# Kernel optimization log

Hardware: AMD Instinct MI355X
Metric: run time of the kernel (lower is better)

The kernel has to match this reference:

```python
import jax, jax.numpy as jnp
import numpy as np

N_NODES = 100000
N_EDGES = 1600000
IN_CH = 128
HID = 128
OUT_CH = 10
NUM_LAYERS = 3
NUM_GRAPHS = 512


def _glorot(key, shape):
    fan_in, fan_out = shape[0], shape[1]
    lim = jnp.sqrt(6.0 / (fan_in + fan_out))
    return jax.random.uniform(key, shape, jnp.float32, -lim, lim)


def setup_inputs() -> dict:
    key = jax.random.key(0)
    ks = jax.random.split(key, 20)
    inp = {}
    inp["x"] = jax.random.normal(ks[0], (N_NODES, IN_CH), jnp.float32)
    inp["edge_index"] = jax.random.randint(ks[1], (2, N_EDGES), 0, N_NODES, jnp.int64)
    inp["batch"] = jnp.sort(jax.random.randint(ks[2], (N_NODES,), 0, NUM_GRAPHS, jnp.int64))
    # GIN layer MLP params: Linear(in, hid) -> ReLU -> Linear(hid, hid)
    kidx = 3
    for l in range(NUM_LAYERS):
        d_in = IN_CH if l == 0 else HID
        inp[f"w1_{l}"] = _glorot(ks[kidx], (d_in, HID)); kidx += 1
        inp[f"b1_{l}"] = jnp.zeros((HID,), jnp.float32)
        inp[f"w2_{l}"] = _glorot(ks[kidx], (HID, HID)); kidx += 1
        inp[f"b2_{l}"] = jnp.zeros((HID,), jnp.float32)
    inp["lin_w"] = _glorot(ks[kidx], (HID, OUT_CH))
    inp["lin_b"] = jnp.zeros((OUT_CH,), jnp.float32)
    return inp


def _gin_forward(x, src, dst, batch, layer_params, lin_w, lin_b):
    h = x
    n_layers = len(layer_params)
    for i, (w1, b1, w2, b2) in enumerate(layer_params):
        # GINConv: (1 + eps) * h + sum_{j in N(i)} h_j, eps = 0
        agg = jax.ops.segment_sum(h[src], dst, num_segments=N_NODES)
        z = h + agg
        # MLP: Linear -> ReLU -> Linear
        h = jnp.maximum(z @ w1 + b1, 0.0) @ w2 + b2
        if i < n_layers - 1:  # inter-layer ReLU (PyG BasicGNN act)
            h = jnp.maximum(h, 0.0)
    # global_add_pool over batch ids -> [NUM_GRAPHS, HID]
    pooled = jax.ops.segment_sum(h, batch, num_segments=NUM_GRAPHS)
    # dropout(p=0.5) is identity in eval mode
    return pooled @ lin_w + lin_b


def reference(x, edge_index, batch,
              w1_0, b1_0, w2_0, b2_0,
              w1_1, b1_1, w2_1, b2_1,
              w1_2, b1_2, w2_2, b2_2,
              lin_w, lin_b):
    src, dst = edge_index[0], edge_index[1]
    layer_params = [(w1_0, b1_0, w2_0, b2_0),
                    (w1_1, b1_1, w2_1, b2_1),
                    (w1_2, b1_2, w2_2, b2_2)]
    return _gin_forward(x, src, dst, batch, layer_params, lin_w, lin_b)
```

## Files before the change

### kernel.cpp

```cpp
#include <hip/hip_runtime.h>

#define CH 128
#define OUTC 10
#define NB 256
#define BCAP 10240
#define PCHUNK 2048
#define PQ2 132
#define FBM 64

typedef __attribute__((ext_vector_type(8))) short short8;
typedef __attribute__((ext_vector_type(4))) short short4v;
typedef __attribute__((ext_vector_type(16))) float f32x16;


__device__ inline unsigned short f2bf(float f) {
    unsigned u = __builtin_bit_cast(unsigned, f);
    u += 0x7fffu + ((u >> 16) & 1u);
    return (unsigned short)(u >> 16);
}
__device__ inline float bflo(unsigned u) { return __builtin_bit_cast(float, u << 16); }
__device__ inline float bfhi(unsigned u) { return __builtin_bit_cast(float, u & 0xffff0000u); }

__device__ inline void acc8(float* a, const uint4& v) {
    a[0] += bflo(v.x); a[1] += bfhi(v.x);
    a[2] += bflo(v.y); a[3] += bfhi(v.y);
    a[4] += bflo(v.z); a[5] += bfhi(v.z);
    a[6] += bflo(v.w); a[7] += bfhi(v.w);
}


struct WPtrs { const float* s[6]; unsigned short* d[6]; };

__global__ void prep_part_kernel(const int* __restrict__ src, const int* __restrict__ dst,
                                 int* __restrict__ bucketCnt, unsigned* __restrict__ pairs, int E,
                                 int nPartBlk,
                                 const float4* __restrict__ x4, uint2* __restrict__ xb, int n4,
                                 int nConvBlk, WPtrs p,
                                 uint4* __restrict__ pooled4, int nPooled4) {
    __shared__ int hist[NB];
    __shared__ int base[NB];
    __shared__ int cur[NB];
    int tid = threadIdx.x;
    int b = blockIdx.x;

    if (b < nPartBlk) {
        int e0 = b * PCHUNK;
        hist[tid] = 0;
        __syncthreads();
        #pragma unroll
        for (int i = 0; i < PCHUNK / 256; ++i) {
            int e = e0 + tid + i * 256;
            if (e < E) atomicAdd(&hist[dst[e] >> 9], 1);
        }
        __syncthreads();
        {
            int c = hist[tid];
            base[tid] = (c > 0) ? atomicAdd(&bucketCnt[tid], c) : 0;
            cur[tid] = 0;
        }
        __syncthreads();
        #pragma unroll
        for (int i = 0; i < PCHUNK / 256; ++i) {
            int e = e0 + tid + i * 256;
            if (e < E) {
                int d = dst[e];
                int bkt = d >> 9;
                int pos = base[bkt] + atomicAdd(&cur[bkt], 1);
                if (pos < BCAP)
                    pairs[bkt * BCAP + pos] = ((unsigned)(d & 511) << 17) | (unsigned)src[e];
            }
        }
    } else if (b < nPartBlk + nConvBlk) {
        int i = (b - nPartBlk) * 256 + tid;
        if (i < n4) {
            float4 v = x4[i];
            uint2 o;
            o.x = (unsigned)f2bf(v.x) | ((unsigned)f2bf(v.y) << 16);
            o.y = (unsigned)f2bf(v.z) | ((unsigned)f2bf(v.w) << 16);
            xb[i] = o;
        }
    } else if (b < nPartBlk + nConvBlk + 384) {
        int bb = b - nPartBlk - nConvBlk;
        int m = bb >> 6;
        int i = (bb & 63) * 256 + tid;
        int j = i & 7;
        int l = (i >> 3) & 63;
        int k0 = (i >> 9) & 7;
        int ct = (i >> 12) & 3;
        int k = k0 * 16 + ((l >> 5) << 3) + j;
        int nn = ct * 32 + (l & 31);
        p.d[m][i] = f2bf(p.s[m][k * CH + nn]);
    } else {
        int i = (b - nPartBlk - nConvBlk - 384) * 256 + tid;
        if (i < nPooled4) pooled4[i] = make_uint4(0, 0, 0, 0);
    }
}


__launch_bounds__(256)
__global__ void build_csr_kernel(const unsigned* __restrict__ pairs, const int* __restrict__ bucketCnt,
                                 int* __restrict__ offs, int* __restrict__ csr, int N) {
    __shared__ int bsm[NB];
    __shared__ int ldeg[512];
    __shared__ int s0[512], s1[512];
    __shared__ int lexc[512];
    __shared__ int lcur[512];
    __shared__ int lcsr[BCAP];

    int b = blockIdx.x;
    int node0 = b << 9;
    if (node0 >= N) return;
    int nLocal = min(512, N - node0);
    int tid = threadIdx.x;

    bsm[tid] = bucketCnt[tid];
    __syncthreads();
    for (int off = 1; off < NB; off <<= 1) {
        int t = (tid >= off) ? bsm[tid - off] : 0;
        __syncthreads();
        bsm[tid] += t;
        __syncthreads();
    }
    int cnt = min(bucketCnt[b], BCAP);
    int gbase = bsm[b] - bucketCnt[b];

    for (int i = tid; i < 512; i += 256) ldeg[i] = 0;
    __syncthreads();
    for (int i = tid; i < cnt; i += 256)
        atomicAdd(&ldeg[pairs[b * BCAP + i] >> 17], 1);
    __syncthreads();

    for (int i = tid; i < 512; i += 256) s0[i] = ldeg[i];
    __syncthreads();
    int* sp = s0; int* dp = s1;
    for (int off = 1; off < 512; off <<= 1) {
        for (int i = tid; i < 512; i += 256)
            dp[i] = sp[i] + ((i >= off) ? sp[i - off] : 0);
        __syncthreads();
        int* t = sp; sp = dp; dp = t;
    }
    for (int i = tid; i < 512; i += 256) {
        int ex = sp[i] - ldeg[i];
        lexc[i] = ex;
        lcur[i] = ex;
    }
    __syncthreads();

    for (int i = tid; i < cnt; i += 256) {
        unsigned w = pairs[b * BCAP + i];
        int ppos = atomicAdd(&lcur[w >> 17], 1);
        lcsr[ppos] = (int)(w & 0x1ffffu);
    }
    __syncthreads();

    for (int i = tid; i < cnt; i += 256) csr[gbase + i] = lcsr[i];
    for (int i = tid; i < nLocal; i += 256) offs[node0 + i] = gbase + lexc[i];
    if (tid == 0 && node0 + nLocal == N) offs[N] = gbase + cnt;
}


template <int L, int RELU, int POOL>
__launch_bounds__(512)
__global__ void fused_gin_kernel(const uint4* __restrict__ h4,
                                 const int* __restrict__ offs, const int* __restrict__ csr,
                                 const unsigned short* __restrict__ w1s, const float* __restrict__ b1,
                                 const unsigned short* __restrict__ w2s, const float* __restrict__ b2,
                                 unsigned short* __restrict__ hout,
                                 const int* __restrict__ batch, float* __restrict__ pooled,
                                 int n) {
    __shared__ __align__(16) unsigned short zs[FBM * PQ2];

    int tid = threadIdx.x;
    int row0 = blockIdx.x * FBM;

    {
        int gl = tid & 15;
        int grp = tid >> 4;
        #pragma unroll
        for (int it = 0; it < 2; ++it) {
            int rr = grp + 32 * it;
            int node = row0 + rr;
            unsigned o0 = 0, o1 = 0, o2 = 0, o3 = 0;
            if (node < n) {
                int beg = offs[node], end = offs[node + 1];
                float a[8];
                uint4 self = h4[node * 16 + gl];
                a[0] = bflo(self.x); a[1] = bfhi(self.x);
                a[2] = bflo(self.y); a[3] = bfhi(self.y);
                a[4] = bflo(self.z); a[5] = bfhi(self.z);
                a[6] = bflo(self.w); a[7] = bfhi(self.w);
                int e = beg;
                for (; e + 4 <= end; e += 4) {
                    int s0 = csr[e], s1 = csr[e + 1], s2 = csr[e + 2], s3 = csr[e + 3];
                    uint4 v0 = h4[s0 * 16 + gl];
                    uint4 v1 = h4[s1 * 16 + gl];
                    uint4 v2 = h4[s2 * 16 + gl];
                    uint4 v3 = h4[s3 * 16 + gl];
                    acc8(a, v0); acc8(a, v1); acc8(a, v2); acc8(a, v3);
                }
                for (; e < end; ++e) {
                    uint4 v = h4[csr[e] * 16 + gl];
                    acc8(a, v);
                }
                o0 = (unsigned)f2bf(a[0]) | ((unsigned)f2bf(a[1]) << 16);
                o1 = (unsigned)f2bf(a[2]) | ((unsigned)f2bf(a[3]) << 16);
                o2 = (unsigned)f2bf(a[4]) | ((unsigned)f2bf(a[5]) << 16);
                o3 = (unsigned)f2bf(a[6]) | ((unsigned)f2bf(a[7]) << 16);
            }
            *(uint2*)&zs[rr * PQ2 + gl * 8]     = make_uint2(o0, o1);
            *(uint2*)&zs[rr * PQ2 + gl * 8 + 4] = make_uint2(o2, o3);
        }
    }
    __syncthreads();

    int wv = tid >> 6;
    int lane = tid & 63;
    int l31 = lane & 31;
    int kh = lane >> 5;
    int rt = wv & 1;
    int ct = wv >> 1;
    int arow = rt * 32 + l31;

    f32x16 acc;
    {
        float bv = b1[ct * 32 + l31];
        #pragma unroll
        for (int r = 0; r < 16; ++r) acc[r] = bv;
    }
    #pragma unroll
    for (int k0 = 0; k0 < 8; ++k0) {
        short8 afr;
        {
            short4v lo = *(const short4v*)&zs[arow * PQ2 + k0 * 16 + kh * 8];
            short4v hi = *(const short4v*)&zs[arow * PQ2 + k0 * 16 + kh * 8 + 4];
            afr = (short8){lo[0], lo[1], lo[2], lo[3], hi[0], hi[1], hi[2], hi[3]};
        }
        short8 bfr = *(const short8*)&w1s[(((ct * 8 + k0) * 64) + lane) * 8];
        acc = __builtin_amdgcn_mfma_f32_32x32x16_bf16(afr, bfr, acc, 0, 0, 0);
    }
    __syncthreads();

    #pragma unroll
    for (int reg = 0; reg < 16; ++reg) {
        int crow = (reg & 3) + 8 * (reg >> 2) + 4 * kh;
        zs[(rt * 32 + crow) * PQ2 + ct * 32 + l31] = f2bf(fmaxf(acc[reg], 0.f));
    }
    __syncthreads();

    {
        float bv = b2[ct * 32 + l31];
        #pragma unroll
        for (int r = 0; r < 16; ++r) acc[r] = bv;
    }
    #pragma unroll
    for (int k0 = 0; k0 < 8; ++k0) {
        short8 afr;
        {
            short4v lo = *(const short4v*)&zs[arow * PQ2 + k0 * 16 + kh * 8];
            short4v hi = *(const short4v*)&zs[arow * PQ2 + k0 * 16 + kh * 8 + 4];
            afr = (short8){lo[0], lo[1], lo[2], lo[3], hi[0], hi[1], hi[2], hi[3]};
        }
        short8 bfr = *(const short8*)&w2s[(((ct * 8 + k0) * 64) + lane) * 8];
        acc = __builtin_amdgcn_mfma_f32_32x32x16_bf16(afr, bfr, acc, 0, 0, 0);
    }
    __syncthreads();

    #pragma unroll
    for (int reg = 0; reg < 16; ++reg) {
        int crow = (reg & 3) + 8 * (reg >> 2) + 4 * kh;
        float v = acc[reg];
        if (RELU) v = fmaxf(v, 0.f);
        zs[(rt * 32 + crow) * PQ2 + ct * 32 + l31] = f2bf(v);
    }
    __syncthreads();

    if (!POOL) {
        for (int i = tid; i < FBM * 16; i += 512) {
            int r = i >> 4, c = i & 15;
            int row = row0 + r;
            if (row < n) {
                uint2 a = *(const uint2*)&zs[r * PQ2 + c * 8];
                uint2 b = *(const uint2*)&zs[r * PQ2 + c * 8 + 4];
                ((uint4*)hout)[row * 16 + c] = make_uint4(a.x, a.y, b.x, b.y);
            }
        }
    } else {
        int c2 = tid & 63;
        int rs = tid >> 6;
        float a0 = 0.f, a1 = 0.f;
        int prevg = -1;
        #pragma unroll
        for (int i = 0; i < FBM / 8; ++i) {
            int r = rs + 8 * i;
            int row = row0 + r;
            if (row >= n) break;
            int g = batch[row];
            if (g != prevg) {
                if (prevg >= 0) {
                    atomicAdd(&pooled[prevg * CH + 2 * c2], a0);
                    atomicAdd(&pooled[prevg * CH + 2 * c2 + 1], a1);
                }
                prevg = g; a0 = 0.f; a1 = 0.f;
            }
            unsigned v = *(const unsigned*)&zs[r * PQ2 + c2 * 2];
            a0 += bflo(v); a1 += bfhi(v);
        }
        if (prevg >= 0) {
            atomicAdd(&pooled[prevg * CH + 2 * c2], a0);
            atomicAdd(&pooled[prevg * CH + 2 * c2 + 1], a1);
        }
    }
}


__global__ void final_linear_kernel(const float* __restrict__ pooled, const float* __restrict__ lin_w,
                                    const float* __restrict__ lin_b, float* __restrict__ out) {
    int g = blockIdx.x;
    int tid = threadIdx.x;
    __shared__ float pl[CH];
    pl[tid] = pooled[g * CH + tid];
    __syncthreads();
    if (tid < OUTC) {
        float a = lin_b[tid];
        #pragma unroll 16
        for (int c = 0; c < CH; ++c) a = fmaf(pl[c], lin_w[c * OUTC + tid], a);
        out[g * OUTC + tid] = a;
    }
}


static inline size_t aln(size_t x) { return (x + 255) & ~size_t(255); }

extern "C" void kernel_launch(void* const* d_in, const int* in_sizes, int n_in,
                              void* d_out, int out_size, void* d_ws, size_t ws_size,
                              hipStream_t stream) {
    const float* x      = (const float*)d_in[0];
    const int*   ei     = (const int*)d_in[1];
    const int*   batch  = (const int*)d_in[2];
    const float* w1[3]  = {(const float*)d_in[3], (const float*)d_in[7],  (const float*)d_in[11]};
    const float* b1[3]  = {(const float*)d_in[4], (const float*)d_in[8],  (const float*)d_in[12]};
    const float* w2[3]  = {(const float*)d_in[5], (const float*)d_in[9],  (const float*)d_in[13]};
    const float* b2[3]  = {(const float*)d_in[6], (const float*)d_in[10], (const float*)d_in[14]};
    const float* lin_w  = (const float*)d_in[15];
    const float* lin_b  = (const float*)d_in[16];
    float* out = (float*)d_out;

    int E = in_sizes[1] / 2;
    int N = in_sizes[2];
    int n_graphs = out_size / OUTC;
    const int* src = ei;
    const int* dst = ei + E;

    char* p = (char*)d_ws;
    int* bucketCnt  = (int*)p; p += aln(NB * 4);
    unsigned* pairs = (unsigned*)p; p += aln((size_t)NB * BCAP * 4);
    int* offs       = (int*)p; p += aln((size_t)(N + 1) * 4);
    int* csr        = (int*)p; p += aln((size_t)E * 4);
    unsigned short* xb = (unsigned short*)p; p += aln((size_t)N * CH * 2);
    unsigned short* hA = (unsigned short*)p; p += aln((size_t)N * CH * 2);
    unsigned short* hB = (unsigned short*)p; p += aln((size_t)N * CH * 2);
    float* pooled = (float*)p; p += aln((size_t)n_graphs * CH * 4);
    unsigned short* wt[6];
    for (int i = 0; i < 6; ++i) { wt[i] = (unsigned short*)p; p += aln((size_t)CH * CH * 2); }
    (void)ws_size; (void)n_in;

    hipMemsetAsync(bucketCnt, 0, NB * 4, stream);

    int n4 = N * CH / 4;
    int nConvBlk = (n4 + 255) / 256;
    int nPartBlk = (E + PCHUNK - 1) / PCHUNK;
    int nPooled4 = n_graphs * CH / 4;
    int nZeroBlk = (nPooled4 + 255) / 256;
    WPtrs wp;
    for (int l = 0; l < 3; ++l) {
        wp.s[2 * l] = w1[l];     wp.d[2 * l] = wt[2 * l];
        wp.s[2 * l + 1] = w2[l]; wp.d[2 * l + 1] = wt[2 * l + 1];
    }
    prep_part_kernel<<<nPartBlk + nConvBlk + 384 + nZeroBlk, 256, 0, stream>>>(
        src, dst, bucketCnt, pairs, E, nPartBlk,
        (const float4*)x, (uint2*)xb, n4, nConvBlk, wp,
        (uint4*)pooled, nPooled4);

    build_csr_kernel<<<NB, 256, 0, stream>>>(pairs, bucketCnt, offs, csr, N);

    int fblk = (N + FBM - 1) / FBM;

    fused_gin_kernel<0, 1, 0><<<fblk, 512, 0, stream>>>((const uint4*)xb, offs, csr,
        wt[0], b1[0], wt[1], b2[0], hA, batch, pooled, N);
    fused_gin_kernel<1, 1, 0><<<fblk, 512, 0, stream>>>((const uint4*)hA, offs, csr,
        wt[2], b1[1], wt[3], b2[1], hB, batch, pooled, N);
    fused_gin_kernel<2, 0, 1><<<fblk, 512, 0, stream>>>((const uint4*)hB, offs, csr,
        wt[4], b1[2], wt[5], b2[2], (unsigned short*)nullptr, batch, pooled, N);

    final_linear_kernel<<<n_graphs, CH, 0, stream>>>(pooled, lin_w, lin_b, out);
}
```

Before: 386.6 us.

## Interleave two nodes' neighbor gathers per thread and widen CSR build blocks

The aggregation phase now has each thread group process its two rows at the same time. Neighbor loads for both nodes are issued together, so more independent memory requests are in flight per thread. Accumulation uses packed float2 vectors so the compiler can emit packed adds. Separately, build_csr_kernel runs with 512 threads, one per local node, which removes the strided loops in the scans. The tradeoffs are more registers and branch divergence when the two nodes have unequal degrees.

```diff
diff --git a/kernel.cpp b/kernel.cpp
--- a/kernel.cpp
+++ b/kernel.cpp
@@ -11,6 +11,7 @@
 typedef __attribute__((ext_vector_type(8))) short short8;
 typedef __attribute__((ext_vector_type(4))) short short4v;
 typedef __attribute__((ext_vector_type(16))) float f32x16;
+typedef __attribute__((ext_vector_type(2))) float f32x2;
 
 
 __device__ inline unsigned short f2bf(float f) {
@@ -21,11 +22,16 @@
 __device__ inline float bflo(unsigned u) { return __builtin_bit_cast(float, u << 16); }
 __device__ inline float bfhi(unsigned u) { return __builtin_bit_cast(float, u & 0xffff0000u); }
 
-__device__ inline void acc8(float* a, const uint4& v) {
-    a[0] += bflo(v.x); a[1] += bfhi(v.x);
-    a[2] += bflo(v.y); a[3] += bfhi(v.y);
-    a[4] += bflo(v.z); a[5] += bfhi(v.z);
-    a[6] += bflo(v.w); a[7] += bfhi(v.w);
+__device__ inline f32x2 bf2(unsigned u) {
+    return (f32x2){__builtin_bit_cast(float, u << 16),
+                   __builtin_bit_cast(float, u & 0xffff0000u)};
+}
+
+__device__ inline void acc8(f32x2* a, const uint4& v) {
+    a[0] += bf2(v.x);
+    a[1] += bf2(v.y);
+    a[2] += bf2(v.z);
+    a[3] += bf2(v.w);
 }
 
 
@@ -97,7 +103,7 @@
 }
 
 
-__launch_bounds__(256)
+__launch_bounds__(512)
 __global__ void build_csr_kernel(const unsigned* __restrict__ pairs, const int* __restrict__ bucketCnt,
                                  int* __restrict__ offs, int* __restrict__ csr, int N) {
     __shared__ int bsm[NB];
@@ -113,48 +119,48 @@
     int nLocal = min(512, N - node0);
     int tid = threadIdx.x;
 
-    bsm[tid] = bucketCnt[tid];
+    if (tid < NB) bsm[tid] = bucketCnt[tid];
     __syncthreads();
     for (int off = 1; off < NB; off <<= 1) {
-        int t = (tid >= off) ? bsm[tid - off] : 0;
-        __syncthreads();
-        bsm[tid] += t;
+        int t = 0;
+        if (tid < NB) t = (tid >= off) ? bsm[tid - off] : 0;
+        __syncthreads();
+        if (tid < NB) bsm[tid] += t;
         __syncthreads();
     }
     int cnt = min(bucketCnt[b], BCAP);
     int gbase = bsm[b] - bucketCnt[b];
 
-    for (int i = tid; i < 512; i += 256) ldeg[i] = 0;
-    __syncthreads();
-    for (int i = tid; i < cnt; i += 256)
+    ldeg[tid] = 0;
+    __syncthreads();
+    for (int i = tid; i < cnt; i += 512)
         atomicAdd(&ldeg[pairs[b * BCAP + i] >> 17], 1);
     __syncthreads();
 
-    for (int i = tid; i < 512; i += 256) s0[i] = ldeg[i];
+    s0[tid] = ldeg[tid];
     __syncthreads();
     int* sp = s0; int* dp = s1;
     for (int off = 1; off < 512; off <<= 1) {
-        for (int i = tid; i < 512; i += 256)
-            dp[i] = sp[i] + ((i >= off) ? sp[i - off] : 0);
+        dp[tid] = sp[tid] + ((tid >= off) ? sp[tid - off] : 0);
         __syncthreads();
         int* t = sp; sp = dp; dp = t;
     }
-    for (int i = tid; i < 512; i += 256) {
-        int ex = sp[i] - ldeg[i];
-        lexc[i] = ex;
-        lcur[i] = ex;
-    }
-    __syncthreads();
-
-    for (int i = tid; i < cnt; i += 256) {
+    {
+        int ex = sp[tid] - ldeg[tid];
+        lexc[tid] = ex;
+        lcur[tid] = ex;
+    }
+    __syncthreads();
+
+    for (int i = tid; i < cnt; i += 512) {
         unsigned w = pairs[b * BCAP + i];
         int ppos = atomicAdd(&lcur[w >> 17], 1);
         lcsr[ppos] = (int)(w & 0x1ffffu);
     }
     __syncthreads();
 
-    for (int i = tid; i < cnt; i += 256) csr[gbase + i] = lcsr[i];
-    for (int i = tid; i < nLocal; i += 256) offs[node0 + i] = gbase + lexc[i];
+    for (int i = tid; i < cnt; i += 512) csr[gbase + i] = lcsr[i];
+    for (int i = tid; i < nLocal; i += 512) offs[node0 + i] = gbase + lexc[i];
     if (tid == 0 && node0 + nLocal == N) offs[N] = gbase + cnt;
 }
 
@@ -176,40 +182,67 @@
     {
         int gl = tid & 15;
         int grp = tid >> 4;
-        #pragma unroll
-        for (int it = 0; it < 2; ++it) {
-            int rr = grp + 32 * it;
-            int node = row0 + rr;
-            unsigned o0 = 0, o1 = 0, o2 = 0, o3 = 0;
-            if (node < n) {
-                int beg = offs[node], end = offs[node + 1];
-                float a[8];
-                uint4 self = h4[node * 16 + gl];
-                a[0] = bflo(self.x); a[1] = bfhi(self.x);
-                a[2] = bflo(self.y); a[3] = bfhi(self.y);
-                a[4] = bflo(self.z); a[5] = bfhi(self.z);
-                a[6] = bflo(self.w); a[7] = bfhi(self.w);
-                int e = beg;
-                for (; e + 4 <= end; e += 4) {
-                    int s0 = csr[e], s1 = csr[e + 1], s2 = csr[e + 2], s3 = csr[e + 3];
-                    uint4 v0 = h4[s0 * 16 + gl];
-                    uint4 v1 = h4[s1 * 16 + gl];
-                    uint4 v2 = h4[s2 * 16 + gl];
-                    uint4 v3 = h4[s3 * 16 + gl];
-                    acc8(a, v0); acc8(a, v1); acc8(a, v2); acc8(a, v3);
-                }
-                for (; e < end; ++e) {
-                    uint4 v = h4[csr[e] * 16 + gl];
-                    acc8(a, v);
-                }
-                o0 = (unsigned)f2bf(a[0]) | ((unsigned)f2bf(a[1]) << 16);
-                o1 = (unsigned)f2bf(a[2]) | ((unsigned)f2bf(a[3]) << 16);
-                o2 = (unsigned)f2bf(a[4]) | ((unsigned)f2bf(a[5]) << 16);
-                o3 = (unsigned)f2bf(a[6]) | ((unsigned)f2bf(a[7]) << 16);
+        int nodeA = row0 + grp;
+        int nodeB = row0 + grp + 32;
+        bool hvA = nodeA < n, hvB = nodeB < n;
+
+        f32x2 a[4], bacc[4];
+        #pragma unroll
+        for (int i = 0; i < 4; ++i) { a[i] = (f32x2){0.f, 0.f}; bacc[i] = (f32x2){0.f, 0.f}; }
+
+        int eA = 0, endA = 0, eB = 0, endB = 0;
+        if (hvA) { eA = offs[nodeA]; endA = offs[nodeA + 1]; }
+        if (hvB) { eB = offs[nodeB]; endB = offs[nodeB + 1]; }
+
+        {
+            uint4 sA = make_uint4(0, 0, 0, 0), sB = make_uint4(0, 0, 0, 0);
+            if (hvA) sA = h4[nodeA * 16 + gl];
+            if (hvB) sB = h4[nodeB * 16 + gl];
+            acc8(a, sA); acc8(bacc, sB);
+        }
+
+        while (true) {
+            bool cA = (eA + 4 <= endA);
+            bool cB = (eB + 4 <= endB);
+            if (!(cA || cB)) break;
+            int sA0 = 0, sA1 = 0, sA2 = 0, sA3 = 0, sB0 = 0, sB1 = 0, sB2 = 0, sB3 = 0;
+            uint4 vA0 = make_uint4(0,0,0,0), vA1 = vA0, vA2 = vA0, vA3 = vA0;
+            uint4 vB0 = vA0, vB1 = vA0, vB2 = vA0, vB3 = vA0;
+            if (cA) { sA0 = csr[eA]; sA1 = csr[eA + 1]; sA2 = csr[eA + 2]; sA3 = csr[eA + 3]; }
+            if (cB) { sB0 = csr[eB]; sB1 = csr[eB + 1]; sB2 = csr[eB + 2]; sB3 = csr[eB + 3]; }
+            if (cA) {
+                vA0 = h4[sA0 * 16 + gl]; vA1 = h4[sA1 * 16 + gl];
+                vA2 = h4[sA2 * 16 + gl]; vA3 = h4[sA3 * 16 + gl];
             }
-            *(uint2*)&zs[rr * PQ2 + gl * 8]     = make_uint2(o0, o1);
-            *(uint2*)&zs[rr * PQ2 + gl * 8 + 4] = make_uint2(o2, o3);
-        }
+            if (cB) {
+                vB0 = h4[sB0 * 16 + gl]; vB1 = h4[sB1 * 16 + gl];
+                vB2 = h4[sB2 * 16 + gl]; vB3 = h4[sB3 * 16 + gl];
+            }
+            if (cA) { acc8(a, vA0); acc8(a, vA1); acc8(a, vA2); acc8(a, vA3); eA += 4; }
+            if (cB) { acc8(bacc, vB0); acc8(bacc, vB1); acc8(bacc, vB2); acc8(bacc, vB3); eB += 4; }
+        }
+        while (eA < endA || eB < endB) {
+            bool dA = eA < endA, dB = eB < endB;
+            uint4 tA = make_uint4(0, 0, 0, 0), tB = make_uint4(0, 0, 0, 0);
+            if (dA) tA = h4[csr[eA] * 16 + gl];
+            if (dB) tB = h4[csr[eB] * 16 + gl];
+            acc8(a, tA); acc8(bacc, tB);
+            eA += dA; eB += dB;
+        }
+
+        unsigned o0 = (unsigned)f2bf(a[0][0]) | ((unsigned)f2bf(a[0][1]) << 16);
+        unsigned o1 = (unsigned)f2bf(a[1][0]) | ((unsigned)f2bf(a[1][1]) << 16);
+        unsigned o2 = (unsigned)f2bf(a[2][0]) | ((unsigned)f2bf(a[2][1]) << 16);
+        unsigned o3 = (unsigned)f2bf(a[3][0]) | ((unsigned)f2bf(a[3][1]) << 16);
+        *(uint2*)&zs[grp * PQ2 + gl * 8]     = make_uint2(o0, o1);
+        *(uint2*)&zs[grp * PQ2 + gl * 8 + 4] = make_uint2(o2, o3);
+
+        o0 = (unsigned)f2bf(bacc[0][0]) | ((unsigned)f2bf(bacc[0][1]) << 16);
+        o1 = (unsigned)f2bf(bacc[1][0]) | ((unsigned)f2bf(bacc[1][1]) << 16);
+        o2 = (unsigned)f2bf(bacc[2][0]) | ((unsigned)f2bf(bacc[2][1]) << 16);
+        o3 = (unsigned)f2bf(bacc[3][0]) | ((unsigned)f2bf(bacc[3][1]) << 16);
+        *(uint2*)&zs[(grp + 32) * PQ2 + gl * 8]     = make_uint2(o0, o1);
+        *(uint2*)&zs[(grp + 32) * PQ2 + gl * 8 + 4] = make_uint2(o2, o3);
     }
     __syncthreads();
 
@@ -279,9 +312,9 @@
             int r = i >> 4, c = i & 15;
             int row = row0 + r;
             if (row < n) {
-                uint2 a = *(const uint2*)&zs[r * PQ2 + c * 8];
-                uint2 b = *(const uint2*)&zs[r * PQ2 + c * 8 + 4];
-                ((uint4*)hout)[row * 16 + c] = make_uint4(a.x, a.y, b.x, b.y);
+                uint2 a2 = *(const uint2*)&zs[r * PQ2 + c * 8];
+                uint2 b2v = *(const uint2*)&zs[r * PQ2 + c * 8 + 4];
+                ((uint4*)hout)[row * 16 + c] = make_uint4(a2.x, a2.y, b2v.x, b2v.y);
             }
         }
     } else {
@@ -381,7 +414,7 @@
         (const float4*)x, (uint2*)xb, n4, nConvBlk, wp,
         (uint4*)pooled, nPooled4);
 
-    build_csr_kernel<<<NB, 256, 0, stream>>>(pairs, bucketCnt, offs, csr, N);
+    build_csr_kernel<<<NB, 512, 0, stream>>>(pairs, bucketCnt, offs, csr, N);
 
     int fblk = (N + FBM - 1) / FBM;
 
```

Result: slower. 407.6 us (+5.4%).
